# Performance work log

Measured on AMD Instinct MI355X. Metric: run time of the kernel, lower is better.

## Reference

```python
import jax, jax.numpy as jnp
import numpy as np

N_CLOUDS = 16
N_PTS = 2048
K = 5            # spline kernel_size per dim
KC = K ** 3      # 125 kernel weights
BITS = np.array([[i & 1, (i >> 1) & 1, (i >> 2) & 1] for i in range(8)])  # degree-1 B-spline corners


def _radius_edges_np(pos, batch, r, max_nb=32):
    # brute-force radius graph, up to max_nb nearest neighbors within r, no self loops
    srcs, tgts = [], []
    for c in np.unique(batch):
        ids = np.where(batch == c)[0]
        P = pos[ids]
        D = np.linalg.norm(P[:, None, :] - P[None, :, :], axis=-1).astype(np.float32)
        np.fill_diagonal(D, np.inf)
        D[D > r] = np.inf
        order = np.argsort(D, axis=1)[:, :max_nb]
        valid = np.isfinite(np.take_along_axis(D, order, axis=1))
        tgt_loc = np.broadcast_to(np.arange(len(ids))[:, None], order.shape)
        srcs.append(ids[order[valid]])
        tgts.append(ids[tgt_loc[valid]])
    return np.concatenate(srcs).astype(np.int32), np.concatenate(tgts).astype(np.int32)


def _fps_np(pos, batch, ratio):
    out = []
    for c in np.unique(batch):
        ids = np.where(batch == c)[0]
        P = pos[ids]
        m = int(round(ratio * len(ids)))
        sel = [0]
        d = np.linalg.norm(P - P[0], axis=1)
        for _ in range(m - 1):
            i = int(d.argmax())
            sel.append(i)
            d = np.minimum(d, np.linalg.norm(P - P[i], axis=1))
        out.append(ids[np.array(sel)])
    return np.concatenate(out).astype(np.int32)


def setup_inputs() -> dict:
    rng = np.random.default_rng(0)
    pos = rng.random((N_CLOUDS * N_PTS, 3)).astype(np.float32)
    batch = np.repeat(np.arange(N_CLOUDS), N_PTS).astype(np.int32)

    src1, tgt1 = _radius_edges_np(pos, batch, 0.2)
    idx1 = _fps_np(pos, batch, 0.5)
    pos2, batch2 = pos[idx1], batch[idx1]
    src2, tgt2 = _radius_edges_np(pos2, batch2, 0.4)
    idx2 = _fps_np(pos2, batch2, 0.25)
    pos3, batch3 = pos2[idx2], batch2[idx2]
    src3, tgt3 = _radius_edges_np(pos3, batch3, 1.0)

    def p(shape, scale=0.1):
        return (rng.standard_normal(shape) * scale).astype(np.float32)

    inp = {
        'pos': jnp.asarray(pos), 'batch': jnp.asarray(batch),
        'src1': jnp.asarray(src1), 'tgt1': jnp.asarray(tgt1),
        'src2': jnp.asarray(src2), 'tgt2': jnp.asarray(tgt2),
        'src3': jnp.asarray(src3), 'tgt3': jnp.asarray(tgt3),
        'idx1': jnp.asarray(idx1), 'idx2': jnp.asarray(idx2),
        'W1': jnp.asarray(p((KC, 1, 64))),  'R1': jnp.asarray(p((1, 64))),   'b1': jnp.zeros((64,), jnp.float32),
        'W2': jnp.asarray(p((KC, 64, 64))), 'R2': jnp.asarray(p((64, 64))),  'b2': jnp.zeros((64,), jnp.float32),
        'W3': jnp.asarray(p((KC, 64, 128))),'R3': jnp.asarray(p((64, 128))), 'b3': jnp.zeros((128,), jnp.float32),
        'lw1': jnp.asarray(p((128, 256))), 'lb1': jnp.zeros((256,), jnp.float32),
        'lw2': jnp.asarray(p((256, 256))), 'lb2': jnp.zeros((256,), jnp.float32),
        'lw3': jnp.asarray(p((256, 10))),  'lb3': jnp.zeros((10,), jnp.float32),
    }
    return inp


def _pseudo(pos, src, tgt, r):
    return jnp.clip((pos[tgt] - pos[src]) / (2.0 * r) + 0.5, 0.0, 1.0)


def _spline_conv(x, pseudo, src, tgt, n, W, R, b):
    # SplineConv: degree-1 open B-spline basis, mean aggregation, root weight + bias
    Cin = x.shape[1]
    v = pseudo * (K - 1)                  # [E,3]
    bot = jnp.floor(v)
    frac = v - bot                        # [E,3]
    boti = bot.astype(jnp.int32)
    xj = x[src]                           # [E,Cin]
    A = jnp.zeros((n * KC, Cin), x.dtype)
    for s in range(8):                    # 8 nonzero basis products per edge
        bits = BITS[s]
        w = jnp.where(bits == 1, frac, 1.0 - frac).prod(-1)     # [E]
        idx = jnp.clip(boti + bits, 0, K - 1)                   # [E,3]
        wi = idx[:, 0] + K * idx[:, 1] + K * K * idx[:, 2]      # [E]
        A = A.at[tgt * KC + wi].add(w[:, None] * xj)
    A = A.reshape(n, KC, Cin)             # per-node per-kernel accumulated features
    msg = jnp.einsum('nkc,kco->no', A, W)
    deg = jax.ops.segment_sum(jnp.ones(tgt.shape[0], x.dtype), tgt, num_segments=n)
    msg = msg / jnp.maximum(deg, 1.0)[:, None]
    return msg + x @ R + b


def reference(pos, batch, src1, tgt1, src2, tgt2, src3, tgt3, idx1, idx2,
              W1, R1, b1, W2, R2, b2, W3, R3, b3,
              lw1, lb1, lw2, lb2, lw3, lb3):
    n1 = pos.shape[0]
    x = jnp.ones((n1, 1), pos.dtype)
    x = jax.nn.elu(_spline_conv(x, _pseudo(pos, src1, tgt1, 0.2), src1, tgt1, n1, W1, R1, b1))
    x, pos2 = x[idx1], pos[idx1]
    n2 = pos2.shape[0]
    x = jax.nn.elu(_spline_conv(x, _pseudo(pos2, src2, tgt2, 0.4), src2, tgt2, n2, W2, R2, b2))
    x, pos3 = x[idx2], pos2[idx2]
    n3 = pos3.shape[0]
    x = jax.nn.elu(_spline_conv(x, _pseudo(pos3, src3, tgt3, 1.0), src3, tgt3, n3, W3, R3, b3))
    batch3 = batch[idx1][idx2]
    num = jax.ops.segment_sum(x, batch3, num_segments=N_CLOUDS)
    cnt = jax.ops.segment_sum(jnp.ones(n3, x.dtype), batch3, num_segments=N_CLOUDS)
    g = num / jnp.maximum(cnt, 1.0)[:, None]          # global_mean_pool [16,128]
    h = jax.nn.elu(g @ lw1 + lb1)
    h = jax.nn.elu(h @ lw2 + lb2)
    # dropout is identity in eval mode
    logits = h @ lw3 + lb3
    return jax.nn.log_softmax(logits, axis=-1)
```

## Files before the change

kernel.cpp:

```cpp
#include <hip/hip_runtime.h>
#include <hip/hip_bf16.h>
#include <math.h>

#define KDIM 5
#define KC 125
#define KPAD 8192
#define EPB 32
#define NSPLIT 8
#define SSTR 40
#define XSTR 40
#define H1STR 40
#define MAXCHUNK 8192

typedef short bf16x8 __attribute__((ext_vector_type(8)));
typedef float f32x4 __attribute__((ext_vector_type(4)));

__device__ __forceinline__ float elu_f(float x) { return x > 0.f ? x : (expf(x) - 1.f); }

__device__ __forceinline__ void fadd_atomic(float* p, float v) {
    unsafeAtomicAdd(p, v);
}

__device__ __forceinline__ unsigned short f2bf(float x) {
    union { float f; unsigned u; } v; v.f = x;
    unsigned r = (v.u + 0x7FFFu + ((v.u >> 16) & 1u)) >> 16;
    return (unsigned short)r;
}

__device__ __forceinline__ void gll16(const unsigned short* g, unsigned short* l) {
    __builtin_amdgcn_global_load_lds(
        (const __attribute__((address_space(1))) unsigned int*)g,
        (__attribute__((address_space(3))) unsigned int*)l, 16, 0, 0);
}

__device__ __forceinline__ void spline_scatter(
    const float* __restrict__ posL, int s, int node, float rinv2, int sinkrow,
    unsigned short* __restrict__ S, int stride, int ecol)
{
    float p0 = fminf(fmaxf((posL[node*3+0] - posL[s*3+0]) * rinv2 + 0.5f, 0.f), 1.f);
    float p1 = fminf(fmaxf((posL[node*3+1] - posL[s*3+1]) * rinv2 + 0.5f, 0.f), 1.f);
    float p2 = fminf(fmaxf((posL[node*3+2] - posL[s*3+2]) * rinv2 + 0.5f, 0.f), 1.f);
    float v0 = p0 * (KDIM - 1), v1 = p1 * (KDIM - 1), v2 = p2 * (KDIM - 1);
    int b0 = (int)floorf(v0), b1 = (int)floorf(v1), b2 = (int)floorf(v2);
    float f0 = v0 - (float)b0, f1 = v1 - (float)b1, f2 = v2 - (float)b2;
    #pragma unroll
    for (int sb = 0; sb < 8; sb++) {
        int i0 = sb & 1, i1 = (sb >> 1) & 1, i2 = (sb >> 2) & 1;
        float w = (i0 ? f0 : 1.f - f0) * (i1 ? f1 : 1.f - f1) * (i2 ? f2 : 1.f - f2);
        int k0 = min(b0 + i0, KDIM - 1), k1 = min(b1 + i1, KDIM - 1), k2 = min(b2 + i2, KDIM - 1);
        int wi = k0 + KDIM * k1 + KDIM * KDIM * k2;
        if (w == 0.f) wi = sinkrow;
        S[wi * stride + ecol] = f2bf(w);
    }
}

__device__ __forceinline__ void rowptr_seg(const int* __restrict__ tgt, int E, int n,
                                           int* __restrict__ rowptr, int e)
{
    if (e < E) {
        int t = tgt[e];
        int p = (e == 0) ? -1 : tgt[e - 1];
        for (int v = p + 1; v <= t; v++) rowptr[v] = e;
    } else {
        int p = tgt[E - 1];
        for (int v = p + 1; v <= n; v++) rowptr[v] = E;
    }
}

__global__ void pre_kernel(
    const float* __restrict__ pos, const int* __restrict__ idx1, const int* __restrict__ idx2,
    int n2, int n3,
    float* __restrict__ pos2, float* __restrict__ pos3,
    const int* __restrict__ tgt1, int E1, int n1, int* __restrict__ rp1,
    const int* __restrict__ tgt2, int E2, int* __restrict__ rp2,
    const int* __restrict__ tgt3, int E3, int* __restrict__ rp3,
    const int* __restrict__ batch, int* __restrict__ cid, float* __restrict__ cnt)
{
    int i = blockIdx.x * blockDim.x + threadIdx.x;
    int w0 = n2 * 3, w1 = w0 + n3 * 3;
    int e0 = w1 + E1 + 1, e1 = e0 + E2 + 1, e2 = e1 + E3 + 1, e3 = e2 + n3;
    if (i < w0) {
        int r = i / 3, d = i - r * 3;
        pos2[i] = pos[idx1[r] * 3 + d];
    } else if (i < w1) {
        int j = i - w0;
        int r = j / 3, d = j - r * 3;
        pos3[j] = pos[idx1[idx2[r]] * 3 + d];
    } else if (i < e0) {
        rowptr_seg(tgt1, E1, n1, rp1, i - w1);
    } else if (i < e1) {
        rowptr_seg(tgt2, E2, n2, rp2, i - e0);
    } else if (i < e2) {
        rowptr_seg(tgt3, E3, n3, rp3, i - e1);
    } else if (i < e3) {
        int j = i - e2;
        int cl = batch[idx1[idx2[j]]];
        cid[j] = cl;
        int lane = threadIdx.x & 63;
        #pragma unroll
        for (int c = 0; c < 16; c++) {
            unsigned long long m = __ballot(cl == c);
            if (m != 0ULL && lane == __ffsll((long long)m) - 1)
                fadd_atomic(&cnt[c], (float)__popcll(m));
        }
    }
}

__global__ __launch_bounds__(256) void wtT_kernel(
    const float* __restrict__ W1, const float* __restrict__ R1, unsigned short* __restrict__ WfT1,
    const float* __restrict__ W2, const float* __restrict__ R2, unsigned short* __restrict__ WfT2,
    const float* __restrict__ W3, const float* __restrict__ R3, unsigned short* __restrict__ WfT3)
{
    __shared__ unsigned short L[64 * 65];
    int bt = blockIdx.x;
    const float *W, *R;
    unsigned short* WfT;
    int COUT, kpad, krows, cin, ntk;
    if (bt < 2)        { W = W1; R = R1; WfT = WfT1; COUT = 64;  kpad = 128;  krows = KC;      cin = 1;  ntk = 2;   }
    else if (bt < 130) { W = W2; R = R2; WfT = WfT2; COUT = 64;  kpad = KPAD; krows = KC * 64; cin = 64; ntk = 128; bt -= 2;   }
    else               { W = W3; R = R3; WfT = WfT3; COUT = 128; kpad = KPAD; krows = KC * 64; cin = 64; ntk = 128; bt -= 130; }
    int kt = (bt % ntk) * 64;
    int nt = (bt / ntk) * 64;
    int t = threadIdx.x;
    int ncol = t & 63, rowgrp = t >> 6;
    #pragma unroll
    for (int j = 0; j < 16; j++) {
        int row = j * 4 + rowgrp;
        int k = kt + row;
        int n = nt + ncol;
        float v = 0.f;
        if (k < krows) v = W[(size_t)k * COUT + n];
        else if (k < krows + cin) v = R[(size_t)(k - krows) * COUT + n];
        L[row * 65 + ncol] = f2bf(v);
    }
    __syncthreads();
    int n = nt + (t >> 2);
    int k0 = (t & 3) * 16;
    __attribute__((aligned(16))) unsigned short tmp[16];
    #pragma unroll
    for (int j = 0; j < 16; j++) tmp[j] = L[(k0 + j) * 65 + (t >> 2)];
    *(uint4*)&WfT[(size_t)n * kpad + kt + k0]     = *(uint4*)&tmp[0];
    *(uint4*)&WfT[(size_t)n * kpad + kt + k0 + 8] = *(uint4*)&tmp[8];
}

__global__ __launch_bounds__(256) void histo1_kernel(const float* __restrict__ pos,
                                                     const int* __restrict__ src,
                                                     const int* __restrict__ rowptr,
                                                     float rinv2, int sinkrow,
                                                     unsigned short* __restrict__ Aout)
{
    __shared__ __attribute__((aligned(16))) unsigned short S[4][128 * H1STR];
    int wave = threadIdx.x >> 6, lane = threadIdx.x & 63;
    int node = blockIdx.x * 4 + wave;
    int rs = rowptr[node], re = rowptr[node + 1];
    int deg = re - rs;
    unsigned short* Sw = S[wave];

    for (int i = lane; i < 128 * H1STR / 8; i += 64)
        ((uint4*)Sw)[i] = make_uint4(0, 0, 0, 0);
    __syncthreads();

    if (lane < deg)
        spline_scatter(pos, src[rs + lane], node, rinv2, sinkrow, Sw, H1STR, lane);
    __syncthreads();

    const short one = 0x3F80;
    bf16x8 bones = {one, one, one, one, one, one, one, one};
    int fr = lane & 15, fq = (lane >> 4) * 8;
    f32x4 acc[8];
    #pragma unroll
    for (int tl = 0; tl < 8; tl++) {
        bf16x8 af = *(const bf16x8*)&Sw[(tl * 16 + fr) * H1STR + fq];
        acc[tl] = __builtin_amdgcn_mfma_f32_16x16x32_bf16(
            af, bones, (f32x4){0.f, 0.f, 0.f, 0.f}, 0, 0, 0);
    }

    float invdeg = 1.f / fmaxf((float)deg, 1.f);
    if ((lane & 15) == 0) {
        int rbase = (lane >> 4) * 4;
        #pragma unroll
        for (int tl = 0; tl < 8; tl++)
            #pragma unroll
            for (int r = 0; r < 4; r++) {
                int row = tl * 16 + rbase + r;
                float v = (row < KC) ? acc[tl][r] * invdeg : (row == KC ? 1.f : 0.f);
                Sw[row] = f2bf(v);
            }
    }
    __syncthreads();
    unsigned lo = Sw[2 * lane], hi = Sw[2 * lane + 1];
    ((unsigned*)(Aout + (size_t)node * 128))[lane] = lo | (hi << 16);
}

__global__ __launch_bounds__(256) void buildA_kernel(
    const float* __restrict__ posL, const int* __restrict__ src,
    const int* __restrict__ rowptr, const unsigned short* __restrict__ xbf,
    float rinv2, int sinkrow, int nodeBase, unsigned short* __restrict__ Aout)
{
    __shared__ __attribute__((aligned(16))) unsigned short BUF[8192];
    __shared__ int Es[EPB];
    unsigned short* S  = BUF;
    unsigned short* XT = BUF + 128 * SSTR;
    int node = nodeBase + blockIdx.x;
    int t = threadIdx.x;
    int rs = rowptr[node], re = rowptr[node + 1];
    int ne = re - rs;
    int wave = t >> 6, lane = t & 63;
    int fr = lane & 15, fq = (lane >> 4) * 8;
    int quad = lane >> 4;

    for (int i = t; i < 128 * SSTR / 8; i += 256)
        ((uint4*)S)[i] = make_uint4(0, 0, 0, 0);
    if (ne < EPB)
        for (int i = t; i < 64 * XSTR / 8; i += 256)
            ((uint4*)XT)[i] = make_uint4(0, 0, 0, 0);
    if (t < ne) Es[t] = src[rs + t];
    __syncthreads();

    if (t < ne)
        spline_scatter(posL, Es[t], node, rinv2, sinkrow, S, SSTR, t);
    for (int i = t; i < ne * 64; i += 256) {
        int c = i & 63, el = i >> 6;
        XT[c * XSTR + el] = xbf[(size_t)Es[el] * 64 + c];
    }
    __syncthreads();

    f32x4 acc[2][4];
    #pragma unroll
    for (int i = 0; i < 2; i++)
        #pragma unroll
        for (int j = 0; j < 4; j++) acc[i][j] = (f32x4){0.f, 0.f, 0.f, 0.f};
    #pragma unroll
    for (int i = 0; i < 2; i++) {
        bf16x8 af = *(const bf16x8*)&S[((2 * wave + i) * 16 + fr) * SSTR + fq];
        #pragma unroll
        for (int j = 0; j < 4; j++) {
            bf16x8 bg = *(const bf16x8*)&XT[(j * 16 + fr) * XSTR + fq];
            acc[i][j] = __builtin_amdgcn_mfma_f32_16x16x32_bf16(af, bg, acc[i][j], 0, 0, 0);
        }
    }
    __syncthreads();

    float invdeg = 1.f / fmaxf((float)ne, 1.f);
    #pragma unroll
    for (int i = 0; i < 2; i++) {
        int wibase = (2 * wave + i) * 16 + quad * 4;
        #pragma unroll
        for (int r = 0; r < 4; r++) {
            int wi = wibase + r;
            if (wi < KC) {
                #pragma unroll
                for (int j = 0; j < 4; j++)
                    BUF[wi * 64 + j * 16 + fr] = f2bf(acc[i][j][r] * invdeg);
            }
        }
    }
    if (t < 64) BUF[8000 + t] = xbf[(size_t)node * 64 + t];
    else if (t < 192) BUF[8000 + t] = 0;
    __syncthreads();

    uint4* out4 = (uint4*)(Aout + (size_t)blockIdx.x * KPAD);
    const uint4* b4 = (const uint4*)BUF;
    #pragma unroll
    for (int k = 0; k < 4; k++) out4[t + k * 256] = b4[t + k * 256];
}

#define LDSOFF(row, colsh) (((row) << 6) + ((colsh) ^ (((row) & 7) << 3)))
__global__ __launch_bounds__(256) void gemm_kernel(const unsigned short* __restrict__ A,
                                                   const unsigned short* __restrict__ BT,
                                                   int Mrows, int COUT, int Ksz, int lda,
                                                   float* __restrict__ P)
{
    __shared__ __attribute__((aligned(16))) unsigned short As[2 * 64 * 64];
    __shared__ __attribute__((aligned(16))) unsigned short Bs[2 * 64 * 64];
    int t = threadIdx.x;
    int mblk = blockIdx.x * 64, nblk = blockIdx.y * 64;
    int kBase = blockIdx.z * Ksz;

    int wave = t >> 6, lane = t & 63;
    int r0 = (wave << 3) + (lane >> 3);
    int ccx = (lane & 7) ^ (r0 & 7);
    const unsigned short* ApB = A + (size_t)(mblk + r0) * lda + kBase + (ccx << 3);
    const unsigned short* BpB = BT + (size_t)(nblk + r0) * lda + kBase + (ccx << 3);
    size_t rstep32 = (size_t)32 * lda;

    int mw = (wave & 1) * 32, nw = (wave >> 1) * 32;
    int fr = lane & 15;
    int fq = (lane >> 4) * 8;

    f32x4 acc[2][2];
    #pragma unroll
    for (int i = 0; i < 2; i++)
        #pragma unroll
        for (int j = 0; j < 2; j++) acc[i][j] = (f32x4){0.f, 0.f, 0.f, 0.f};

    gll16(ApB,           &As[(wave << 9)]);
    gll16(ApB + rstep32, &As[2048 + (wave << 9)]);
    gll16(BpB,           &Bs[(wave << 9)]);
    gll16(BpB + rstep32, &Bs[2048 + (wave << 9)]);

    int ktiles = Ksz / 64;
    for (int kt = 0; kt < ktiles; kt++) {
        int cur = (kt & 1) * 4096;
        if (kt + 1 < ktiles) {
            int nxt = ((kt + 1) & 1) * 4096;
            const unsigned short* Apn = ApB + (kt + 1) * 64;
            const unsigned short* Bpn = BpB + (kt + 1) * 64;
            gll16(Apn,           &As[nxt + (wave << 9)]);
            gll16(Apn + rstep32, &As[nxt + 2048 + (wave << 9)]);
            gll16(Bpn,           &Bs[nxt + (wave << 9)]);
            gll16(Bpn + rstep32, &Bs[nxt + 2048 + (wave << 9)]);
            asm volatile("s_waitcnt vmcnt(4)" ::: "memory");
        } else {
            asm volatile("s_waitcnt vmcnt(0)" ::: "memory");
        }
        __builtin_amdgcn_s_barrier();
        #pragma unroll
        for (int ks = 0; ks < 2; ks++) {
            bf16x8 af0 = *(const bf16x8*)&As[cur + LDSOFF(mw + fr,      ks * 32 + fq)];
            bf16x8 af1 = *(const bf16x8*)&As[cur + LDSOFF(mw + 16 + fr, ks * 32 + fq)];
            bf16x8 bg0 = *(const bf16x8*)&Bs[cur + LDSOFF(nw + fr,      ks * 32 + fq)];
            bf16x8 bg1 = *(const bf16x8*)&Bs[cur + LDSOFF(nw + 16 + fr, ks * 32 + fq)];
            acc[0][0] = __builtin_amdgcn_mfma_f32_16x16x32_bf16(af0, bg0, acc[0][0], 0, 0, 0);
            acc[0][1] = __builtin_amdgcn_mfma_f32_16x16x32_bf16(af0, bg1, acc[0][1], 0, 0, 0);
            acc[1][0] = __builtin_amdgcn_mfma_f32_16x16x32_bf16(af1, bg0, acc[1][0], 0, 0, 0);
            acc[1][1] = __builtin_amdgcn_mfma_f32_16x16x32_bf16(af1, bg1, acc[1][1], 0, 0, 0);
        }
        if (kt + 1 < ktiles)
            __builtin_amdgcn_s_barrier();
    }
    float* Pz = P + (size_t)blockIdx.z * Mrows * COUT;
    int crow = (lane >> 4) * 4, ccol = lane & 15;
    #pragma unroll
    for (int i = 0; i < 2; i++)
        #pragma unroll
        for (int j = 0; j < 2; j++) {
            int m0 = mblk + mw + i * 16 + crow;
            int n0 = nblk + nw + j * 16 + ccol;
            #pragma unroll
            for (int r = 0; r < 4; r++)
                Pz[(size_t)(m0 + r) * COUT + n0] = acc[i][j][r];
        }
}

__global__ void combine2_kernel(const float* __restrict__ P, const float* __restrict__ b,
                                int Mrows, int NS, unsigned short* __restrict__ xout)
{
    int i = blockIdx.x * blockDim.x + threadIdx.x;
    int total = Mrows * 64;
    if (i >= total) return;
    float s = 0.f;
    for (int z = 0; z < NS; z++) s += P[(size_t)z * total + i];
    xout[i] = f2bf(elu_f(s + b[i & 63]));
}

__global__ void combine1g_kernel(const float* __restrict__ P, const float* __restrict__ b,
                                 const int* __restrict__ idx1, int n2,
                                 unsigned short* __restrict__ x2in)
{
    int i = blockIdx.x * blockDim.x + threadIdx.x;
    if (i >= n2 * 64) return;
    int r = i >> 6, c = i & 63;
    x2in[i] = f2bf(elu_f(P[(size_t)idx1[r] * 64 + c] + b[c]));
}

__global__ void combinepool_kernel(const float* __restrict__ P, const float* __restrict__ b,
                                   const int* __restrict__ cid, int cs, int Mrows, int NS,
                                   float* __restrict__ gnum)
{
    int i = blockIdx.x * blockDim.x + threadIdx.x;
    int total = Mrows * 128;
    if (i >= total) return;
    int r = i >> 7, c = i & 127;
    float s = 0.f;
    for (int z = 0; z < NS; z++) s += P[(size_t)z * total + i];
    float v = elu_f(s + b[c]);
    fadd_atomic(&gnum[cid[cs + r] * 128 + c], v);
}

__global__ void xgather_kernel(const unsigned short* __restrict__ x_src,
                               const int* __restrict__ idx,
                               int n, unsigned short* __restrict__ x_dst)
{
    int tid = blockIdx.x * blockDim.x + threadIdx.x;
    if (tid >= n * 64) return;
    int i = tid >> 6, c = tid & 63;
    x_dst[tid] = x_src[(size_t)idx[i] * 64 + c];
}

__global__ void mlp_kernel(const float* __restrict__ gnum, const float* __restrict__ cnt,
                           const float* __restrict__ lw1, const float* __restrict__ lb1,
                           const float* __restrict__ lw2, const float* __restrict__ lb2,
                           const float* __restrict__ lw3, const float* __restrict__ lb3,
                           float* __restrict__ out)
{
    __shared__ float gv[128], h1[256], h2[256], lg[10];
    __shared__ float lse_s;
    int cl = blockIdx.x, t = threadIdx.x;
    if (t < 128) gv[t] = gnum[cl * 128 + t] / fmaxf(cnt[cl], 1.f);
    __syncthreads();
    float a = lb1[t];
    for (int c = 0; c < 128; c++) a += gv[c] * lw1[c * 256 + t];
    h1[t] = elu_f(a);
    __syncthreads();
    a = lb2[t];
    for (int c = 0; c < 256; c++) a += h1[c] * lw2[c * 256 + t];
    h2[t] = elu_f(a);
    __syncthreads();
    if (t < 10) {
        a = lb3[t];
        for (int c = 0; c < 256; c++) a += h2[c] * lw3[c * 10 + t];
        lg[t] = a;
    }
    __syncthreads();
    if (t == 0) {
        float m = -1e30f;
        for (int i = 0; i < 10; i++) m = fmaxf(m, lg[i]);
        float s = 0.f;
        for (int i = 0; i < 10; i++) s += expf(lg[i] - m);
        lse_s = m + logf(s);
    }
    __syncthreads();
    if (t < 10) out[cl * 10 + t] = lg[t] - lse_s;
}

extern "C" void kernel_launch(void* const* d_in, const int* in_sizes, int n_in,
                              void* d_out, int out_size, void* d_ws, size_t ws_size,
                              hipStream_t stream)
{
    const float* pos   = (const float*)d_in[0];
    const int*   batch = (const int*)d_in[1];
    const int*   src1  = (const int*)d_in[2];
    const int*   tgt1  = (const int*)d_in[3];
    const int*   src2  = (const int*)d_in[4];
    const int*   tgt2  = (const int*)d_in[5];
    const int*   src3  = (const int*)d_in[6];
    const int*   tgt3  = (const int*)d_in[7];
    const int*   idx1  = (const int*)d_in[8];
    const int*   idx2  = (const int*)d_in[9];
    const float* W1 = (const float*)d_in[10];
    const float* R1 = (const float*)d_in[11];
    const float* b1 = (const float*)d_in[12];
    const float* W2 = (const float*)d_in[13];
    const float* R2 = (const float*)d_in[14];
    const float* b2 = (const float*)d_in[15];
    const float* W3 = (const float*)d_in[16];
    const float* R3 = (const float*)d_in[17];
    const float* b3 = (const float*)d_in[18];
    const float* lw1 = (const float*)d_in[19];
    const float* lb1 = (const float*)d_in[20];
    const float* lw2 = (const float*)d_in[21];
    const float* lb2 = (const float*)d_in[22];
    const float* lw3 = (const float*)d_in[23];
    const float* lb3 = (const float*)d_in[24];

    int n1 = in_sizes[0] / 3;
    int E1 = in_sizes[2];
    int E2 = in_sizes[4];
    int E3 = in_sizes[6];
    int n2 = in_sizes[8];
    int n3 = in_sizes[9];

    float* ws = (float*)d_ws;
    float* pos2 = ws;
    float* pos3 = pos2 + (size_t)n2 * 3;
    float* gnum = pos3 + (size_t)n3 * 3;
    float* cnt  = gnum + 16 * 128;
    int*   cid  = (int*)(cnt + 16);
    unsigned short* x2o  = (unsigned short*)(cid + ((n3 + 4) & ~3));
    unsigned short* x2in = x2o  + (size_t)n2 * 64;
    unsigned short* x3in = x2in + (size_t)n2 * 64;
    unsigned short* WfT1 = x3in + (size_t)n3 * 64;
    unsigned short* WfT2 = WfT1 + (size_t)64 * 128;
    unsigned short* WfT3 = WfT2 + (size_t)64 * KPAD;
    int*   rp1  = (int*)(WfT3 + (size_t)128 * KPAD);
    int*   rp2  = rp1 + ((n1 + 4) & ~3);
    int*   rp3  = rp2 + ((n2 + 4) & ~3);
    unsigned short* A1buf = (unsigned short*)(rp3 + ((n3 + 4) & ~3));
    float*  P    = (float*)(A1buf + (size_t)n1 * 128);
    unsigned short* Abuf = (unsigned short*)(P + (size_t)8 * 1024 * 1024);

    size_t usedBytes = (size_t)((char*)Abuf - (char*)ws);
    size_t availBytes = ws_size > usedBytes ? ws_size - usedBytes : 0;
    int maxRows = (int)(availBytes / ((size_t)KPAD * 2));
    maxRows &= ~63;
    if (maxRows < 64) maxRows = 64;
    if (maxRows > MAXCHUNK) maxRows = MAXCHUNK;
    int rowsP2 = ((8 * 1024 * 1024) / (NSPLIT * 64)) & ~63;
    int rowsP3 = ((8 * 1024 * 1024) / (NSPLIT * 128)) & ~63;
    int rows2 = min(min(maxRows, rowsP2), n2);
    int rows3 = min(min(maxRows, rowsP3), n3);

    float* out = (float*)d_out;
    int Ksz = KPAD / NSPLIT;

    {
        hipMemsetAsync(gnum, 0, (16 * 128 + 16) * sizeof(float), stream);
        int tot = n2 * 3 + n3 * 3
                + (E1 + 1) + (E2 + 1) + (E3 + 1) + n3;
        pre_kernel<<<(tot + 255) / 256, 256, 0, stream>>>(
            pos, idx1, idx2, n2, n3, pos2, pos3,
            tgt1, E1, n1, rp1, tgt2, E2, rp2, tgt3, E3, rp3,
            batch, cid, cnt);
        wtT_kernel<<<386, 256, 0, stream>>>(W1, R1, WfT1, W2, R2, WfT2, W3, R3, WfT3);
    }

    histo1_kernel<<<n1 / 4, 256, 0, stream>>>(pos, src1, rp1, 2.5f, 126, A1buf);
    {
        dim3 g1(n1 / 64, 1, 1);
        gemm_kernel<<<g1, 256, 0, stream>>>(A1buf, WfT1, n1, 64, 128, 128, P);
        combine1g_kernel<<<(n2 * 64 + 255) / 256, 256, 0, stream>>>(P, b1, idx1, n2, x2in);
    }

    for (int cs = 0; cs < n2; cs += rows2) {
        int cr = min(rows2, n2 - cs);
        buildA_kernel<<<cr, 256, 0, stream>>>(pos2, src2, rp2, x2in, 1.25f, 125, cs, Abuf);
        dim3 grid(cr / 64, 1, NSPLIT);
        gemm_kernel<<<grid, 256, 0, stream>>>(Abuf, WfT2, cr, 64, Ksz, KPAD, P);
        combine2_kernel<<<(cr * 64 + 255) / 256, 256, 0, stream>>>(P, b2, cr, NSPLIT,
                                                                   x2o + (size_t)cs * 64);
    }
    xgather_kernel<<<(n3 * 64 + 255) / 256, 256, 0, stream>>>(x2o, idx2, n3, x3in);

    for (int cs = 0; cs < n3; cs += rows3) {
        int cr = min(rows3, n3 - cs);
        buildA_kernel<<<cr, 256, 0, stream>>>(pos3, src3, rp3, x3in, 0.5f, 125, cs, Abuf);
        dim3 grid(cr / 64, 2, NSPLIT);
        gemm_kernel<<<grid, 256, 0, stream>>>(Abuf, WfT3, cr, 128, Ksz, KPAD, P);
        combinepool_kernel<<<(cr * 128 + 255) / 256, 256, 0, stream>>>(P, b3, cid, cs, cr,
                                                                       NSPLIT, gnum);
    }

    mlp_kernel<<<16, 256, 0, stream>>>(gnum, cnt, lw1, lb1, lw2, lb2, lw3, lb3, out);
}
```

Measured before the change: 348.0 us.

## Replace split-K partial buffers with atomic accumulation and fuse layer-1 epilogue into GEMM

The split-K GEMM now adds its partials straight into a zeroed fp32 accumulator with atomics, instead of writing NSPLIT partial slabs that a separate combine kernel re-reads and sums. The layer-1 GEMM applies bias, ELU and the bf16 conversion in its own epilogue, and the gather then runs on the bf16 output. Dropping the large P buffer also lets the row chunks grow up to the workspace limit, which cuts the number of kernel launches. In exchange it adds memsets for the accumulators, atomic contention, and fp32 summation order that is no longer deterministic.

```diff
diff --git a/kernel.cpp b/kernel.cpp
--- a/kernel.cpp
+++ b/kernel.cpp
@@ -269,7 +269,9 @@
 __global__ __launch_bounds__(256) void gemm_kernel(const unsigned short* __restrict__ A,
                                                    const unsigned short* __restrict__ BT,
                                                    int Mrows, int COUT, int Ksz, int lda,
-                                                   float* __restrict__ P)
+                                                   float* __restrict__ Pacc,
+                                                   unsigned short* __restrict__ outBf,
+                                                   const float* __restrict__ bias)
 {
     __shared__ __attribute__((aligned(16))) unsigned short As[2 * 64 * 64];
     __shared__ __attribute__((aligned(16))) unsigned short Bs[2 * 64 * 64];
@@ -329,53 +331,31 @@
         if (kt + 1 < ktiles)
             __builtin_amdgcn_s_barrier();
     }
-    float* Pz = P + (size_t)blockIdx.z * Mrows * COUT;
     int crow = (lane >> 4) * 4, ccol = lane & 15;
-    #pragma unroll
-    for (int i = 0; i < 2; i++)
-        #pragma unroll
-        for (int j = 0; j < 2; j++) {
-            int m0 = mblk + mw + i * 16 + crow;
-            int n0 = nblk + nw + j * 16 + ccol;
+    if (outBf) {
+        #pragma unroll
+        for (int i = 0; i < 2; i++)
             #pragma unroll
-            for (int r = 0; r < 4; r++)
-                Pz[(size_t)(m0 + r) * COUT + n0] = acc[i][j][r];
-        }
-}
-
-__global__ void combine2_kernel(const float* __restrict__ P, const float* __restrict__ b,
-                                int Mrows, int NS, unsigned short* __restrict__ xout)
-{
-    int i = blockIdx.x * blockDim.x + threadIdx.x;
-    int total = Mrows * 64;
-    if (i >= total) return;
-    float s = 0.f;
-    for (int z = 0; z < NS; z++) s += P[(size_t)z * total + i];
-    xout[i] = f2bf(elu_f(s + b[i & 63]));
-}
-
-__global__ void combine1g_kernel(const float* __restrict__ P, const float* __restrict__ b,
-                                 const int* __restrict__ idx1, int n2,
-                                 unsigned short* __restrict__ x2in)
-{
-    int i = blockIdx.x * blockDim.x + threadIdx.x;
-    if (i >= n2 * 64) return;
-    int r = i >> 6, c = i & 63;
-    x2in[i] = f2bf(elu_f(P[(size_t)idx1[r] * 64 + c] + b[c]));
-}
-
-__global__ void combinepool_kernel(const float* __restrict__ P, const float* __restrict__ b,
-                                   const int* __restrict__ cid, int cs, int Mrows, int NS,
-                                   float* __restrict__ gnum)
-{
-    int i = blockIdx.x * blockDim.x + threadIdx.x;
-    int total = Mrows * 128;
-    if (i >= total) return;
-    int r = i >> 7, c = i & 127;
-    float s = 0.f;
-    for (int z = 0; z < NS; z++) s += P[(size_t)z * total + i];
-    float v = elu_f(s + b[c]);
-    fadd_atomic(&gnum[cid[cs + r] * 128 + c], v);
+            for (int j = 0; j < 2; j++) {
+                int m0 = mblk + mw + i * 16 + crow;
+                int n0 = nblk + nw + j * 16 + ccol;
+                float bv = bias[n0];
+                #pragma unroll
+                for (int r = 0; r < 4; r++)
+                    outBf[(size_t)(m0 + r) * COUT + n0] = f2bf(elu_f(acc[i][j][r] + bv));
+            }
+    } else {
+        #pragma unroll
+        for (int i = 0; i < 2; i++)
+            #pragma unroll
+            for (int j = 0; j < 2; j++) {
+                int m0 = mblk + mw + i * 16 + crow;
+                int n0 = nblk + nw + j * 16 + ccol;
+                #pragma unroll
+                for (int r = 0; r < 4; r++)
+                    fadd_atomic(&Pacc[(size_t)(m0 + r) * COUT + n0], acc[i][j][r]);
+            }
+    }
 }
 
 __global__ void xgather_kernel(const unsigned short* __restrict__ x_src,
@@ -386,6 +366,27 @@
     if (tid >= n * 64) return;
     int i = tid >> 6, c = tid & 63;
     x_dst[tid] = x_src[(size_t)idx[i] * 64 + c];
+}
+
+__global__ void cg23_kernel(const float* __restrict__ x2acc, const float* __restrict__ b,
+                            const int* __restrict__ idx2, int n3,
+                            unsigned short* __restrict__ x3in)
+{
+    int i = blockIdx.x * blockDim.x + threadIdx.x;
+    if (i >= n3 * 64) return;
+    int r = i >> 6, c = i & 63;
+    x3in[i] = f2bf(elu_f(x2acc[(size_t)idx2[r] * 64 + c] + b[c]));
+}
+
+__global__ void combinepool_kernel(const float* __restrict__ x3acc, const float* __restrict__ b,
+                                   const int* __restrict__ cid, int n3,
+                                   float* __restrict__ gnum)
+{
+    int i = blockIdx.x * blockDim.x + threadIdx.x;
+    if (i >= n3 * 128) return;
+    int r = i >> 7, c = i & 127;
+    float v = elu_f(x3acc[i] + b[c]);
+    fadd_atomic(&gnum[cid[r] * 128 + c], v);
 }
 
 __global__ void mlp_kernel(const float* __restrict__ gnum, const float* __restrict__ cnt,
@@ -467,8 +468,10 @@
     float* gnum = pos3 + (size_t)n3 * 3;
     float* cnt  = gnum + 16 * 128;
     int*   cid  = (int*)(cnt + 16);
-    unsigned short* x2o  = (unsigned short*)(cid + ((n3 + 4) & ~3));
-    unsigned short* x2in = x2o  + (size_t)n2 * 64;
+    float* x2acc = (float*)(cid + ((n3 + 4) & ~3));
+    float* x3acc = x2acc + (size_t)n2 * 64;
+    unsigned short* x1bf = (unsigned short*)(x3acc + (size_t)n3 * 128);
+    unsigned short* x2in = x1bf + (size_t)n1 * 64;
     unsigned short* x3in = x2in + (size_t)n2 * 64;
     unsigned short* WfT1 = x3in + (size_t)n3 * 64;
     unsigned short* WfT2 = WfT1 + (size_t)64 * 128;
@@ -477,8 +480,7 @@
     int*   rp2  = rp1 + ((n1 + 4) & ~3);
     int*   rp3  = rp2 + ((n2 + 4) & ~3);
     unsigned short* A1buf = (unsigned short*)(rp3 + ((n3 + 4) & ~3));
-    float*  P    = (float*)(A1buf + (size_t)n1 * 128);
-    unsigned short* Abuf = (unsigned short*)(P + (size_t)8 * 1024 * 1024);
+    unsigned short* Abuf = A1buf + (size_t)n1 * 128;
 
     size_t usedBytes = (size_t)((char*)Abuf - (char*)ws);
     size_t availBytes = ws_size > usedBytes ? ws_size - usedBytes : 0;
@@ -486,16 +488,16 @@
     maxRows &= ~63;
     if (maxRows < 64) maxRows = 64;
     if (maxRows > MAXCHUNK) maxRows = MAXCHUNK;
-    int rowsP2 = ((8 * 1024 * 1024) / (NSPLIT * 64)) & ~63;
-    int rowsP3 = ((8 * 1024 * 1024) / (NSPLIT * 128)) & ~63;
-    int rows2 = min(min(maxRows, rowsP2), n2);
-    int rows3 = min(min(maxRows, rowsP3), n3);
+    int rows2 = min(maxRows, n2);
+    int rows3 = min(maxRows, n3);
 
     float* out = (float*)d_out;
     int Ksz = KPAD / NSPLIT;
 
     {
         hipMemsetAsync(gnum, 0, (16 * 128 + 16) * sizeof(float), stream);
+        hipMemsetAsync(x2acc, 0, (size_t)n2 * 64 * sizeof(float), stream);
+        hipMemsetAsync(x3acc, 0, (size_t)n3 * 128 * sizeof(float), stream);
         int tot = n2 * 3 + n3 * 3
                 + (E1 + 1) + (E2 + 1) + (E3 + 1) + n3;
         pre_kernel<<<(tot + 255) / 256, 256, 0, stream>>>(
@@ -508,28 +510,28 @@
     histo1_kernel<<<n1 / 4, 256, 0, stream>>>(pos, src1, rp1, 2.5f, 126, A1buf);
     {
         dim3 g1(n1 / 64, 1, 1);
-        gemm_kernel<<<g1, 256, 0, stream>>>(A1buf, WfT1, n1, 64, 128, 128, P);
-        combine1g_kernel<<<(n2 * 64 + 255) / 256, 256, 0, stream>>>(P, b1, idx1, n2, x2in);
+        gemm_kernel<<<g1, 256, 0, stream>>>(A1buf, WfT1, n1, 64, 128, 128,
+                                            nullptr, x1bf, b1);
+        xgather_kernel<<<(n2 * 64 + 255) / 256, 256, 0, stream>>>(x1bf, idx1, n2, x2in);
     }
 
     for (int cs = 0; cs < n2; cs += rows2) {
         int cr = min(rows2, n2 - cs);
         buildA_kernel<<<cr, 256, 0, stream>>>(pos2, src2, rp2, x2in, 1.25f, 125, cs, Abuf);
         dim3 grid(cr / 64, 1, NSPLIT);
-        gemm_kernel<<<grid, 256, 0, stream>>>(Abuf, WfT2, cr, 64, Ksz, KPAD, P);
-        combine2_kernel<<<(cr * 64 + 255) / 256, 256, 0, stream>>>(P, b2, cr, NSPLIT,
-                                                                   x2o + (size_t)cs * 64);
-    }
-    xgather_kernel<<<(n3 * 64 + 255) / 256, 256, 0, stream>>>(x2o, idx2, n3, x3in);
+        gemm_kernel<<<grid, 256, 0, stream>>>(Abuf, WfT2, cr, 64, Ksz, KPAD,
+                                              x2acc + (size_t)cs * 64, nullptr, nullptr);
+    }
+    cg23_kernel<<<(n3 * 64 + 255) / 256, 256, 0, stream>>>(x2acc, b2, idx2, n3, x3in);
 
     for (int cs = 0; cs < n3; cs += rows3) {
         int cr = min(rows3, n3 - cs);
         buildA_kernel<<<cr, 256, 0, stream>>>(pos3, src3, rp3, x3in, 0.5f, 125, cs, Abuf);
         dim3 grid(cr / 64, 2, NSPLIT);
-        gemm_kernel<<<grid, 256, 0, stream>>>(Abuf, WfT3, cr, 128, Ksz, KPAD, P);
-        combinepool_kernel<<<(cr * 128 + 255) / 256, 256, 0, stream>>>(P, b3, cid, cs, cr,
-                                                                       NSPLIT, gnum);
-    }
+        gemm_kernel<<<grid, 256, 0, stream>>>(Abuf, WfT3, cr, 128, Ksz, KPAD,
+                                              x3acc + (size_t)cs * 128, nullptr, nullptr);
+    }
+    combinepool_kernel<<<(n3 * 128 + 255) / 256, 256, 0, stream>>>(x3acc, b3, cid, n3, gnum);
 
     mlp_kernel<<<16, 256, 0, stream>>>(gnum, cnt, lw1, lb1, lw2, lb2, lw3, lb3, out);
 }
```

Result: slower. 399.1 us (+14.7%).
